# Kernel tuning notes

Measured on AMD Instinct MI355X. Metric: run time of the kernel, lower is better.

Reference implementation:

```python
import jax, jax.numpy as jnp
import numpy as np

P, S, C, F, B = 2, 2, 64, 64, 64


def setup_inputs() -> dict:
    key = jax.random.key(0)
    kx, kq, kw = jax.random.split(key, 3)
    X = jax.random.normal(kx, (B, P * S * C * F), dtype=jnp.float32)
    # sparse connection-strength tensor, densified; nonnegative small values
    dbfc = jax.random.uniform(kq, (P, S, C, F, C, F), dtype=jnp.float32) * 0.01
    wV = jax.random.normal(kw, (F, F), dtype=jnp.float32) * (1.0 / np.sqrt(F))
    return {"X": X, "databaseFeatureConnections": dbfc, "wV": wV}


def reference(X, databaseFeatureConnections, wV):
    p, s, c, f = (databaseFeatureConnections.shape[0], databaseFeatureConnections.shape[1],
                  databaseFeatureConnections.shape[2], databaseFeatureConnections.shape[3])
    b = X.shape[0]
    # wV: nn.Linear(f, f, bias=False) -> x @ W.T
    v = (X.reshape(b, p * s * c, f) @ wV.T).reshape(b, p, s, c, f)
    # kqHead.sum(dim=1).sum(dim=2): collapse both feature axes -> [p, s, c, c]
    scores = databaseFeatureConnections.sum(axis=(3, 5))
    weights = jax.nn.softmax(scores, axis=-1)  # [p, s, c, c]
    # per-head bmm: weights[p,s] @ v[:,p,s] -> [b, c, f] per head; heads concatenated
    # along feature dim in (p outer, s inner) order == reshape of [b, c, p, s, f]
    out = jnp.einsum('pscd,bpsdf->bcpsf', weights, v).reshape(b, c, p * s * f)
    # permute(1, 0, 2) -> [c, b, p*s*f]
    return out.transpose(1, 0, 2)
```

## Files before the change

### kernel.cpp

```cpp
#include <hip/hip_runtime.h>
#include <math.h>


typedef float floatx4 __attribute__((ext_vector_type(4)));

__global__ __launch_bounds__(256) void scores_partial_kernel(
    const float* __restrict__ dbfc, float* __restrict__ partials)
{
    const int bid   = blockIdx.x;
    const int slab  = bid >> 3;
    const int chunk = bid & 7;
    const int t     = threadIdx.x;

    const floatx4* src = reinterpret_cast<const floatx4*>(dbfc)
                       + (size_t)slab * 65536 + chunk * 8192 + t;

    floatx4 a0 = (floatx4)0.f, a1 = (floatx4)0.f, a2 = (floatx4)0.f, a3 = (floatx4)0.f;
#pragma unroll 2
    for (int i = 0; i < 32; i += 4) {
        floatx4 v0 = __builtin_nontemporal_load(&src[(i + 0) * 256]);
        floatx4 v1 = __builtin_nontemporal_load(&src[(i + 1) * 256]);
        floatx4 v2 = __builtin_nontemporal_load(&src[(i + 2) * 256]);
        floatx4 v3 = __builtin_nontemporal_load(&src[(i + 3) * 256]);
        a0 += v0;
        a1 += v1;
        a2 += v2;
        a3 += v3;
    }
    float s0 = (a0.x + a0.y) + (a0.z + a0.w);
    float s1 = (a1.x + a1.y) + (a1.z + a1.w);
    float s2 = (a2.x + a2.y) + (a2.z + a2.w);
    float s3 = (a3.x + a3.y) + (a3.z + a3.w);
#pragma unroll
    for (int m = 1; m < 16; m <<= 1) {
        s0 += __shfl_xor(s0, m, 64);
        s1 += __shfl_xor(s1, m, 64);
        s2 += __shfl_xor(s2, m, 64);
        s3 += __shfl_xor(s3, m, 64);
    }
    if ((t & 15) == 0) {
        float* dst = partials + (size_t)chunk * 16384 + slab * 64 + (t >> 4);
        dst[ 0] = s0;
        dst[16] = s1;
        dst[32] = s2;
        dst[48] = s3;
    }
}

__global__ __launch_bounds__(256) void attn_out_kernel(
    const float* __restrict__ X, const float* __restrict__ wV,
    const float* __restrict__ partials, float* __restrict__ out)
{
    const int blk = blockIdx.x;
    const int ps  = blk >> 6;
    const int b   = blk & 63;
    const int t   = threadIdx.x;
    const int tc  = t >> 4;
    const int tf  = t & 15;

    __shared__ float Xs [64][68];
    __shared__ float wVs[64][68];
    __shared__ float Ws [64][68];
    __shared__ float VsT[64][68];

    const float4* xsrc = reinterpret_cast<const float4*>(X + (size_t)b * 16384 + ps * 4096);
    const float4* wsrc = reinterpret_cast<const float4*>(wV);
    const float4* psrc = reinterpret_cast<const float4*>(partials);
#pragma unroll
    for (int idx = t; idx < 1024; idx += 256) {
        int r = idx >> 4, jq = idx & 15, j = jq * 4;
        *reinterpret_cast<float4*>(&Xs [r][j]) = xsrc[idx];
        *reinterpret_cast<float4*>(&wVs[r][j]) = wsrc[idx];
        float4 s = make_float4(0.f, 0.f, 0.f, 0.f);
#pragma unroll
        for (int k = 0; k < 8; ++k) {
            float4 p = psrc[k * 4096 + (ps * 64 + r) * 16 + jq];
            s.x += p.x; s.y += p.y; s.z += p.z; s.w += p.w;
        }
        *reinterpret_cast<float4*>(&Ws [r][j]) = s;
    }
    __syncthreads();

    float acc[4][4] = {};
    for (int f0 = 0; f0 < 64; f0 += 4) {
        float4 xa[4], wv[4];
#pragma unroll
        for (int ci = 0; ci < 4; ++ci)
            xa[ci] = *reinterpret_cast<const float4*>(&Xs[4 * tc + ci][f0]);
#pragma unroll
        for (int fi = 0; fi < 4; ++fi)
            wv[fi] = *reinterpret_cast<const float4*>(&wVs[tf + 16 * fi][f0]);
#pragma unroll
        for (int ci = 0; ci < 4; ++ci)
#pragma unroll
            for (int fi = 0; fi < 4; ++fi)
                acc[ci][fi] += xa[ci].x * wv[fi].x + xa[ci].y * wv[fi].y
                             + xa[ci].z * wv[fi].z + xa[ci].w * wv[fi].w;
    }

    {
        const int row = t >> 2, q = (t & 3) * 16;
        float e[16];
        float mx = -INFINITY;
#pragma unroll
        for (int i = 0; i < 16; ++i) mx = fmaxf(mx, Ws[row][q + i]);
        mx = fmaxf(mx, __shfl_xor(mx, 1, 64));
        mx = fmaxf(mx, __shfl_xor(mx, 2, 64));
        float sum = 0.f;
#pragma unroll
        for (int i = 0; i < 16; ++i) { e[i] = expf(Ws[row][q + i] - mx); sum += e[i]; }
        sum += __shfl_xor(sum, 1, 64);
        sum += __shfl_xor(sum, 2, 64);
        const float rinv = 1.0f / sum;
#pragma unroll
        for (int i = 0; i < 16; ++i) Ws[row][q + i] = e[i] * rinv;
    }

#pragma unroll
    for (int ci = 0; ci < 4; ++ci)
#pragma unroll
        for (int fi = 0; fi < 4; ++fi)
            VsT[tf + 16 * fi][4 * tc + ci] = acc[ci][fi];
    __syncthreads();

    float o[4][4] = {};
    for (int d = 0; d < 64; d += 4) {
        float4 wa[4], va[4];
#pragma unroll
        for (int ci = 0; ci < 4; ++ci)
            wa[ci] = *reinterpret_cast<const float4*>(&Ws[4 * tc + ci][d]);
#pragma unroll
        for (int fi = 0; fi < 4; ++fi)
            va[fi] = *reinterpret_cast<const float4*>(&VsT[tf + 16 * fi][d]);
#pragma unroll
        for (int ci = 0; ci < 4; ++ci)
#pragma unroll
            for (int fi = 0; fi < 4; ++fi)
                o[ci][fi] += wa[ci].x * va[fi].x + wa[ci].y * va[fi].y
                           + wa[ci].z * va[fi].z + wa[ci].w * va[fi].w;
    }

#pragma unroll
    for (int ci = 0; ci < 4; ++ci) {
        const int c = 4 * tc + ci;
        float* orow = out + ((size_t)c * 64 + b) * 256 + ps * 64;
#pragma unroll
        for (int fi = 0; fi < 4; ++fi)
            orow[tf + 16 * fi] = o[ci][fi];
    }
}

extern "C" void kernel_launch(void* const* d_in, const int* in_sizes, int n_in,
                              void* d_out, int out_size, void* d_ws, size_t ws_size,
                              hipStream_t stream)
{
    const float* X    = (const float*)d_in[0];
    const float* dbfc = (const float*)d_in[1];
    const float* wV   = (const float*)d_in[2];
    float* out        = (float*)d_out;
    float* partials   = (float*)d_ws;

    scores_partial_kernel<<<2048, 256, 0, stream>>>(dbfc, partials);
    attn_out_kernel<<<256, 256, 0, stream>>>(X, wV, partials, out);
}
```

Baseline: 54.78 us.

## Split attention output kernel across four query-row quarters to raise block count

The attention kernel now launches four times as many blocks, each handling 16 of the 64 output rows for a given (ps, b). Each block still recomputes the full 64x64 V projection, but only loads and softmaxes its 16 score rows. VsT reuses the Xs shared buffer, which cuts shared memory per block. This trades redundant V matmul work and X/wV loads for more parallelism across the GPU's CUs (256 blocks previously).

```diff
diff --git a/kernel.cpp b/kernel.cpp
--- a/kernel.cpp
+++ b/kernel.cpp
@@ -52,7 +52,8 @@
     const float* __restrict__ partials, float* __restrict__ out)
 {
     const int blk = blockIdx.x;
-    const int ps  = blk >> 6;
+    const int cq  = blk >> 8;
+    const int ps  = (blk >> 6) & 3;
     const int b   = blk & 63;
     const int t   = threadIdx.x;
     const int tc  = t >> 4;
@@ -60,24 +61,26 @@
 
     __shared__ float Xs [64][68];
     __shared__ float wVs[64][68];
-    __shared__ float Ws [64][68];
-    __shared__ float VsT[64][68];
+    __shared__ float Ws [16][68];
 
     const float4* xsrc = reinterpret_cast<const float4*>(X + (size_t)b * 16384 + ps * 4096);
     const float4* wsrc = reinterpret_cast<const float4*>(wV);
     const float4* psrc = reinterpret_cast<const float4*>(partials);
 #pragma unroll
     for (int idx = t; idx < 1024; idx += 256) {
-        int r = idx >> 4, jq = idx & 15, j = jq * 4;
+        int r = idx >> 4, j = (idx & 15) * 4;
         *reinterpret_cast<float4*>(&Xs [r][j]) = xsrc[idx];
         *reinterpret_cast<float4*>(&wVs[r][j]) = wsrc[idx];
+    }
+    {
+        int r = t >> 4, jq = t & 15;
         float4 s = make_float4(0.f, 0.f, 0.f, 0.f);
 #pragma unroll
         for (int k = 0; k < 8; ++k) {
-            float4 p = psrc[k * 4096 + (ps * 64 + r) * 16 + jq];
+            float4 p = psrc[k * 4096 + (ps * 64 + cq * 16 + r) * 16 + jq];
             s.x += p.x; s.y += p.y; s.z += p.z; s.w += p.w;
         }
-        *reinterpret_cast<float4*>(&Ws [r][j]) = s;
+        *reinterpret_cast<float4*>(&Ws[r][jq * 4]) = s;
     }
     __syncthreads();
 
@@ -98,7 +101,7 @@
                              + xa[ci].z * wv[fi].z + xa[ci].w * wv[fi].w;
     }
 
-    {
+    if (t < 64) {
         const int row = t >> 2, q = (t & 3) * 16;
         float e[16];
         float mx = -INFINITY;
@@ -115,7 +118,9 @@
 #pragma unroll
         for (int i = 0; i < 16; ++i) Ws[row][q + i] = e[i] * rinv;
     }
+    __syncthreads();
 
+    float (*VsT)[68] = Xs;
 #pragma unroll
     for (int ci = 0; ci < 4; ++ci)
 #pragma unroll
@@ -123,30 +128,25 @@
             VsT[tf + 16 * fi][4 * tc + ci] = acc[ci][fi];
     __syncthreads();
 
-    float o[4][4] = {};
+    float o[4] = {};
     for (int d = 0; d < 64; d += 4) {
-        float4 wa[4], va[4];
-#pragma unroll
-        for (int ci = 0; ci < 4; ++ci)
-            wa[ci] = *reinterpret_cast<const float4*>(&Ws[4 * tc + ci][d]);
+        float4 wa = *reinterpret_cast<const float4*>(&Ws[tc][d]);
+        float4 va[4];
 #pragma unroll
         for (int fi = 0; fi < 4; ++fi)
             va[fi] = *reinterpret_cast<const float4*>(&VsT[tf + 16 * fi][d]);
 #pragma unroll
-        for (int ci = 0; ci < 4; ++ci)
-#pragma unroll
-            for (int fi = 0; fi < 4; ++fi)
-                o[ci][fi] += wa[ci].x * va[fi].x + wa[ci].y * va[fi].y
-                           + wa[ci].z * va[fi].z + wa[ci].w * va[fi].w;
+        for (int fi = 0; fi < 4; ++fi)
+            o[fi] += wa.x * va[fi].x + wa.y * va[fi].y
+                   + wa.z * va[fi].z + wa.w * va[fi].w;
     }
 
-#pragma unroll
-    for (int ci = 0; ci < 4; ++ci) {
-        const int c = 4 * tc + ci;
+    {
+        const int c = cq * 16 + tc;
         float* orow = out + ((size_t)c * 64 + b) * 256 + ps * 64;
 #pragma unroll
         for (int fi = 0; fi < 4; ++fi)
-            orow[tf + 16 * fi] = o[ci][fi];
+            orow[tf + 16 * fi] = o[fi];
     }
 }
 
@@ -161,5 +161,5 @@
     float* partials   = (float*)d_ws;
 
     scores_partial_kernel<<<2048, 256, 0, stream>>>(dbfc, partials);
-    attn_out_kernel<<<256, 256, 0, stream>>>(X, wV, partials, out);
+    attn_out_kernel<<<1024, 256, 0, stream>>>(X, wV, partials, out);
 }
```

Result: slower. 59.88 us (+9.3%).
